# Kernel optimization log

Measured on AMD Instinct MI355X. Metric: run time of the kernel, lower is better.

Reference implementation:

```python
import jax, jax.numpy as jnp
import numpy as np

NUM_USERS = 100000
NUM_ITEMS = 50000
NUM_NODES = NUM_USERS + NUM_ITEMS
EMB = 64
NUM_EDGES = 2000000
BATCH = 16384


def setup_inputs() -> dict:
    key = jax.random.key(0)
    ks = jax.random.split(key, 9)

    def xavier(k, shape):
        fan_in, fan_out = shape[-2], shape[-1]
        lim = float(np.sqrt(6.0 / (fan_in + fan_out)))
        return jax.random.uniform(k, shape, jnp.float32, -lim, lim)

    user_table = xavier(ks[0], (NUM_USERS, EMB))
    item_table = xavier(ks[1], (NUM_ITEMS, EMB))
    # gat1: in=64, heads=4, out=64 -> W1 [64, 256]; a1 [4, 128]
    W1 = xavier(ks[2], (EMB, EMB * 4))
    a1 = xavier(ks[3], (4, 2 * EMB))
    # gat2: in=256, heads=1, out=64 -> W2 [256, 64]; a2 [1, 128]
    W2 = xavier(ks[4], (EMB * 4, EMB))
    a2 = xavier(ks[5], (1, 2 * EMB))

    edge_index = jax.random.randint(ks[6], (2, NUM_EDGES), 0, NUM_NODES, dtype=jnp.int32)
    user_ids = jax.random.randint(ks[7], (BATCH,), 0, NUM_USERS, dtype=jnp.int32)
    item_ids = jax.random.randint(ks[8], (BATCH,), 0, NUM_ITEMS, dtype=jnp.int32)
    return {
        "user_table": user_table, "item_table": item_table,
        "W1": W1, "a1": a1, "W2": W2, "a2": a2,
        "edge_index": edge_index, "user_ids": user_ids, "item_ids": item_ids,
    }


def gat_layer(x, W, a, num_heads, out_features, src, dst, concat):
    n = x.shape[0]
    h = (x @ W).reshape(n, num_heads, out_features)          # [N,H,F]
    # attention score: (cat(h_src,h_dst) * a).sum(-1) == h_src.a_l + h_dst.a_r
    a_l, a_r = a[:, :out_features], a[:, out_features:]
    e_src = jnp.einsum('nhf,hf->nh', h, a_l)                 # [N,H]
    e_dst = jnp.einsum('nhf,hf->nh', h, a_r)
    att = e_src[src] + e_dst[dst]                            # [E,H]
    att = jnp.where(att > 0, att, 0.2 * att)                 # LeakyReLU(0.2)
    att = jnp.exp(att - jnp.max(att))                        # global max, as in torch code
    att_sum = jax.ops.segment_sum(att, dst, num_segments=n)  # [N,H]
    att = att / (att_sum[dst] + 1e-8)
    msg = att[:, :, None] * h[src]                           # [E,H,F]
    out = jax.ops.segment_sum(msg, dst, num_segments=n)      # [N,H,F]
    return out.reshape(n, -1) if concat else out.mean(axis=1)


def reference(user_table, item_table, W1, a1, W2, a2, edge_index, user_ids, item_ids):
    src, dst = edge_index[0], edge_index[1]
    all_emb = jnp.concatenate([user_table, item_table], axis=0)  # [N,64]
    h = gat_layer(all_emb, W1, a1, 4, EMB, src, dst, concat=True)  # [N,256]
    h = jax.nn.elu(h)
    h = gat_layer(h, W2, a2, 1, EMB, src, dst, concat=False)       # [N,64]
    h = h + all_emb
    user_emb = h[:NUM_USERS]
    item_emb = h[NUM_USERS:]
    return jnp.sum(user_emb[user_ids] * item_emb[item_ids], axis=1)
```

## Files before the change

### kernel.cpp

```cpp
#include <hip/hip_runtime.h>
#include <cstdint>
#include <cstddef>

#define NUM_USERS 100000
#define NUM_ITEMS 50000
#define NUM_NODES 150000
#define NUM_EDGES 2000000
#define BATCH 16384
#define BSHIFT 8
#define NBUCK ((NUM_NODES + 255) >> BSHIFT)
#define PA_EDGES 8192
#define PA_BLOCKS ((NUM_EDGES + PA_EDGES - 1) / PA_EDGES)
#define NNPAD 150016
#define TBLK (NNPAD / 64)

typedef _Float16 hf8 __attribute__((ext_vector_type(8)));
typedef _Float16 hf4 __attribute__((ext_vector_type(4)));
typedef float fx4 __attribute__((ext_vector_type(4)));

__global__ void flag_kernel(const int* __restrict__ uid, const int* __restrict__ iid,
                            int* __restrict__ nodelist, int* __restrict__ bcnt,
                            int* __restrict__ gcnt) {
  int i = blockIdx.x * blockDim.x + threadIdx.x;
  if (i < NBUCK) bcnt[i] = 0;
  if (i < 2) gcnt[i] = 0;
  if (i < BATCH) {
    nodelist[2 * i] = uid[i];
    nodelist[2 * i + 1] = NUM_USERS + iid[i];
  }
}

__global__ __launch_bounds__(256) void bhist_kernel(const int* __restrict__ dst,
                                                    int* __restrict__ bcnt) {
  __shared__ int bh[NBUCK];
  int t = threadIdx.x;
  for (int u = t; u < NBUCK; u += 256) bh[u] = 0;
  __syncthreads();
  int base = blockIdx.x * PA_EDGES;
#pragma unroll
  for (int u = 0; u < PA_EDGES / 256; ++u) {
    int e = base + u * 256 + t;
    if (e < NUM_EDGES) atomicAdd(&bh[dst[e] >> BSHIFT], 1);
  }
  __syncthreads();
  for (int u = t; u < NBUCK; u += 256) {
    int v = bh[u];
    if (v) atomicAdd(&bcnt[u], v);
  }
}

__global__ void bscan_kernel(const int* __restrict__ bcnt, int* __restrict__ bbase,
                             int* __restrict__ bcursor, int* __restrict__ offsets) {
  __shared__ int sh[1024];
  int t = threadIdx.x;
  int v = (t < NBUCK) ? bcnt[t] : 0;
  sh[t] = v;
  __syncthreads();
  for (int off = 1; off < 1024; off <<= 1) {
    int x = (t >= off) ? sh[t - off] : 0;
    __syncthreads();
    sh[t] += x;
    __syncthreads();
  }
  if (t < NBUCK) {
    bbase[t] = sh[t] - v;
    bcursor[t] = sh[t] - v;
  }
  if (t == NBUCK - 1) {
    bbase[NBUCK] = sh[t];
    offsets[NUM_NODES] = sh[t];
  }
}

__global__ __launch_bounds__(256) void bpart_kernel(const int* __restrict__ src,
                                                    const int* __restrict__ dst,
                                                    int* __restrict__ bcursor,
                                                    int2* __restrict__ ebuf) {
  __shared__ int lcnt[NBUCK];
  __shared__ int lbase[NBUCK];
  int t = threadIdx.x;
  for (int u = t; u < NBUCK; u += 256) lcnt[u] = 0;
  __syncthreads();
  int base = blockIdx.x * PA_EDGES;
#pragma unroll
  for (int u = 0; u < PA_EDGES / 256; ++u) {
    int e = base + u * 256 + t;
    if (e < NUM_EDGES) atomicAdd(&lcnt[dst[e] >> BSHIFT], 1);
  }
  __syncthreads();
  for (int u = t; u < NBUCK; u += 256) {
    int v = lcnt[u];
    lbase[u] = v ? atomicAdd(&bcursor[u], v) : 0;
    lcnt[u] = 0;
  }
  __syncthreads();
#pragma unroll
  for (int u = 0; u < PA_EDGES / 256; ++u) {
    int e = base + u * 256 + t;
    if (e < NUM_EDGES) {
      int d = dst[e];
      int b = d >> BSHIFT;
      int p = lbase[b] + atomicAdd(&lcnt[b], 1);
      ebuf[p] = make_int2(src[e], d);
    }
  }
}

__global__ __launch_bounds__(256) void bcsr_kernel(const int2* __restrict__ ebuf,
                                                   const int* __restrict__ bbase,
                                                   int* __restrict__ offsets,
                                                   int* __restrict__ srcs) {
  __shared__ int ncnt[256];
  __shared__ int sh[256];
  __shared__ int lcur[256];
  int b = blockIdx.x;
  int t = threadIdx.x;
  int node0 = b << BSHIFT;
  int ebeg = bbase[b], eend = bbase[b + 1];
  ncnt[t] = 0;
  __syncthreads();
  for (int i = ebeg + t; i < eend; i += 256)
    atomicAdd(&ncnt[ebuf[i].y - node0], 1);
  __syncthreads();
  int v = ncnt[t];
  sh[t] = v;
  __syncthreads();
  for (int off = 1; off < 256; off <<= 1) {
    int x = (t >= off) ? sh[t - off] : 0;
    __syncthreads();
    sh[t] += x;
    __syncthreads();
  }
  int excl = ebeg + sh[t] - v;
  if (node0 + t < NUM_NODES) offsets[node0 + t] = excl;
  lcur[t] = excl;
  __syncthreads();
  for (int i = ebeg + t; i < eend; i += 256) {
    int2 ed = ebuf[i];
    int p = atomicAdd(&lcur[ed.y - node0], 1);
    srcs[p] = ed.x;
  }
}

__global__ __launch_bounds__(256) void dlist_kernel(
    const int* __restrict__ offsets, int* __restrict__ gcnt,
    int* __restrict__ Ls, int* __restrict__ Lm,
    _Float16* __restrict__ aXhi, _Float16* __restrict__ aXlo) {
  __shared__ int c0, c1, b0, b1;
  int t = threadIdx.x;
  int n = blockIdx.x * 256 + t;
  if (t == 0) { c0 = 0; c1 = 0; }
  __syncthreads();
  int cls = -1, rank = 0;
  if (n < NUM_NODES) {
    int deg = offsets[n + 1] - offsets[n];
    cls = (deg <= 16) ? 0 : 1;
    rank = atomicAdd(cls == 0 ? &c0 : &c1, 1);
  } else if (n < NNPAD) {
    float4 z = make_float4(0.f, 0.f, 0.f, 0.f);
#pragma unroll
    for (int i = 0; i < 32; ++i) {
      ((float4*)(aXhi + (size_t)n * 256))[i] = z;
      ((float4*)(aXlo + (size_t)n * 256))[i] = z;
    }
  }
  __syncthreads();
  if (t == 0) {
    b0 = atomicAdd(&gcnt[0], c0);
    b1 = atomicAdd(&gcnt[1], c1);
  }
  __syncthreads();
  if (cls == 0) Ls[b0 + rank] = n;
  else if (cls == 1) Lm[b1 + rank] = n;
}

__global__ void proj1_kernel(const float* __restrict__ W1, const float* __restrict__ a1,
                             float* __restrict__ w1a, float* __restrict__ w1b) {
  int t = threadIdx.x;
  int h = t >> 6, k = t & 63;
  float sa = 0.f, sb = 0.f;
  for (int f = 0; f < 64; ++f) {
    float w = W1[(size_t)k * 256 + h * 64 + f];
    sa += w * a1[h * 128 + f];
    sb += w * a1[h * 128 + 64 + f];
  }
  w1a[h * 64 + k] = sa;
  w1b[h * 64 + k] = sb;
}

__device__ __forceinline__ const float* row_ptr(int s, const float* __restrict__ ut,
                                                const float* __restrict__ it) {
  return (s < NUM_USERS) ? ut + (size_t)s * 64 : it + (size_t)(s - NUM_USERS) * 64;
}

__device__ __forceinline__ float lrexp(float x) {
  x = x > 0.f ? x : 0.2f * x;
  return __expf(x);
}

__device__ __forceinline__ float wnorm(float w) {
  float sum = w;
#pragma unroll
  for (int off = 32; off; off >>= 1) sum += __shfl_xor(sum, off, 64);
  return w * (1.f / (sum + 1e-8f));
}

__device__ __forceinline__ void fold4(float4& a) {
#pragma unroll
  for (int off = 16; off <= 32; off <<= 1) {
    a.x += __shfl_xor(a.x, off, 64);
    a.y += __shfl_xor(a.y, off, 64);
    a.z += __shfl_xor(a.z, off, 64);
    a.w += __shfl_xor(a.w, off, 64);
  }
}

__device__ __forceinline__ float elu(float x) {
  return x > 0.f ? x : (__expf(x) - 1.f);
}

__device__ __forceinline__ void split4(float4 o, hf4& hv, hf4& lv) {
  float a0 = o.x * 256.f, a1 = o.y * 256.f, a2 = o.z * 256.f, a3 = o.w * 256.f;
  _Float16 h0 = (_Float16)a0, h1 = (_Float16)a1;
  _Float16 h2 = (_Float16)a2, h3 = (_Float16)a3;
  hv[0] = h0; hv[1] = h1; hv[2] = h2; hv[3] = h3;
  lv[0] = (_Float16)(a0 - (float)h0);
  lv[1] = (_Float16)(a1 - (float)h1);
  lv[2] = (_Float16)(a2 - (float)h2);
  lv[3] = (_Float16)(a3 - (float)h3);
}

__device__ __forceinline__ void splitstore(_Float16* __restrict__ hi,
                                           _Float16* __restrict__ lo,
                                           size_t idx, float v) {
  v *= 256.f;
  _Float16 h = (_Float16)v;
  hi[idx] = h;
  lo[idx] = (_Float16)(v - (float)h);
}

__global__ __launch_bounds__(256) void e1g_kernel(
    const float* __restrict__ ut, const float* __restrict__ it,
    const float* __restrict__ w1a, const float* __restrict__ w1b,
    float* __restrict__ e1s, float* __restrict__ e1d) {
  int t = threadIdx.x;
  int wave = t >> 6, lane = t & 63;
  int g = lane >> 4, fl = lane & 15;
  int node = blockIdx.x * 16 + wave * 4 + g;
  bool valid = node < NUM_NODES;
  float4 xv = make_float4(0.f, 0.f, 0.f, 0.f);
  if (valid) xv = *(const float4*)(row_ptr(node, ut, it) + fl * 4);
  float ps[4], pd[4];
#pragma unroll
  for (int h = 0; h < 4; ++h) {
    float4 wa = *(const float4*)(w1a + h * 64 + fl * 4);
    float4 wb = *(const float4*)(w1b + h * 64 + fl * 4);
    ps[h] = xv.x * wa.x + xv.y * wa.y + xv.z * wa.z + xv.w * wa.w;
    pd[h] = xv.x * wb.x + xv.y * wb.y + xv.z * wb.z + xv.w * wb.w;
  }
#pragma unroll
  for (int off = 8; off; off >>= 1) {
#pragma unroll
    for (int h = 0; h < 4; ++h) {
      ps[h] += __shfl_xor(ps[h], off, 16);
      pd[h] += __shfl_xor(pd[h], off, 16);
    }
  }
  if (valid && fl == 0) {
    *(float4*)(e1s + (size_t)node * 4) = make_float4(ps[0], ps[1], ps[2], ps[3]);
    *(float4*)(e1d + (size_t)node * 4) = make_float4(pd[0], pd[1], pd[2], pd[3]);
  }
}

__global__ __launch_bounds__(256) void aggXs_kernel(
    const int* __restrict__ Ls, const int* __restrict__ gcnt,
    const int* __restrict__ offsets, const int* __restrict__ srcs,
    const float* __restrict__ e1s, const float* __restrict__ e1d,
    const float* __restrict__ ut, const float* __restrict__ it,
    _Float16* __restrict__ aXhi, _Float16* __restrict__ aXlo) {
  __shared__ int sS[4][68];
  __shared__ __align__(16) float4 sW[4][68];
  const int t = threadIdx.x;
  const int wave = t >> 6, lane = t & 63;
  const int g = lane >> 4, fl = lane & 15;
  const int cnt = gcnt[0];
  const int widx = blockIdx.x * 16 + wave * 4 + g;
  const int node = (widx < cnt) ? Ls[widx] : -1;

  int beg = 0, deg = 0;
  float4 ed = make_float4(0.f, 0.f, 0.f, 0.f);
  if (node >= 0) {
    beg = offsets[node];
    deg = offsets[node + 1] - beg;
    ed = *(const float4*)(e1d + (size_t)node * 4);
  }
  int s = 0;
  float w0 = 0.f, w1 = 0.f, w2 = 0.f, w3 = 0.f;
  if (fl < deg) {
    s = srcs[beg + fl];
    float4 ev = *(const float4*)(e1s + (size_t)s * 4);
    w0 = lrexp(ev.x + ed.x);
    w1 = lrexp(ev.y + ed.y);
    w2 = lrexp(ev.z + ed.z);
    w3 = lrexp(ev.w + ed.w);
  }
  float t0 = w0, t1 = w1, t2 = w2, t3 = w3;
#pragma unroll
  for (int off = 8; off; off >>= 1) {
    t0 += __shfl_xor(t0, off, 16);
    t1 += __shfl_xor(t1, off, 16);
    t2 += __shfl_xor(t2, off, 16);
    t3 += __shfl_xor(t3, off, 16);
  }
  w0 *= 1.f / (t0 + 1e-8f);
  w1 *= 1.f / (t1 + 1e-8f);
  w2 *= 1.f / (t2 + 1e-8f);
  w3 *= 1.f / (t3 + 1e-8f);
  sS[wave][g * 17 + fl] = s;
  sW[wave][g * 17 + fl] = make_float4(w0, w1, w2, w3);

  int md = deg;
  md = max(md, __shfl_xor(md, 16, 64));
  md = max(md, __shfl_xor(md, 32, 64));

  float4 a0 = make_float4(0.f, 0.f, 0.f, 0.f);
  float4 a1 = a0, a2 = a0, a3 = a0;
#pragma unroll 2
  for (int e = 0; e < md; ++e) {
    int se = sS[wave][g * 17 + e];
    float4 w4 = sW[wave][g * 17 + e];
    float4 xv = *(const float4*)(row_ptr(se, ut, it) + fl * 4);
    a0.x += w4.x * xv.x; a0.y += w4.x * xv.y; a0.z += w4.x * xv.z; a0.w += w4.x * xv.w;
    a1.x += w4.y * xv.x; a1.y += w4.y * xv.y; a1.z += w4.y * xv.z; a1.w += w4.y * xv.w;
    a2.x += w4.z * xv.x; a2.y += w4.z * xv.y; a2.z += w4.z * xv.z; a2.w += w4.z * xv.w;
    a3.x += w4.w * xv.x; a3.y += w4.w * xv.y; a3.z += w4.w * xv.z; a3.w += w4.w * xv.w;
  }
  if (node >= 0) {
    hf4 hv, lv;
    split4(a0, hv, lv);
    *(hf4*)(aXhi + (size_t)node * 256 + 0 * 64 + fl * 4) = hv;
    *(hf4*)(aXlo + (size_t)node * 256 + 0 * 64 + fl * 4) = lv;
    split4(a1, hv, lv);
    *(hf4*)(aXhi + (size_t)node * 256 + 1 * 64 + fl * 4) = hv;
    *(hf4*)(aXlo + (size_t)node * 256 + 1 * 64 + fl * 4) = lv;
    split4(a2, hv, lv);
    *(hf4*)(aXhi + (size_t)node * 256 + 2 * 64 + fl * 4) = hv;
    *(hf4*)(aXlo + (size_t)node * 256 + 2 * 64 + fl * 4) = lv;
    split4(a3, hv, lv);
    *(hf4*)(aXhi + (size_t)node * 256 + 3 * 64 + fl * 4) = hv;
    *(hf4*)(aXlo + (size_t)node * 256 + 3 * 64 + fl * 4) = lv;
  }
}

__global__ __launch_bounds__(256) void aggXm_kernel(
    const int* __restrict__ Lm, const int* __restrict__ gcnt,
    const int* __restrict__ offsets, const int* __restrict__ srcs,
    const float* __restrict__ e1s, const float* __restrict__ e1d,
    const float* __restrict__ ut, const float* __restrict__ it,
    _Float16* __restrict__ aXhi, _Float16* __restrict__ aXlo) {
  int wid = threadIdx.x >> 6, lane = threadIdx.x & 63;
  int idx = blockIdx.x * 4 + wid;
  if (idx >= gcnt[1]) return;
  int node = Lm[idx];
  int beg = offsets[node], end = offsets[node + 1];
  int deg = end - beg;

  float edv0 = e1d[(size_t)node * 4 + 0];
  float edv1 = e1d[(size_t)node * 4 + 1];
  float edv2 = e1d[(size_t)node * 4 + 2];
  float edv3 = e1d[(size_t)node * 4 + 3];

  if (deg <= 64) {
    int s = 0;
    float w0 = 0.f, w1 = 0.f, w2 = 0.f, w3 = 0.f;
    if (lane < deg) {
      s = srcs[beg + lane];
      float4 ev = *(const float4*)(e1s + (size_t)s * 4);
      w0 = lrexp(ev.x + edv0);
      w1 = lrexp(ev.y + edv1);
      w2 = lrexp(ev.z + edv2);
      w3 = lrexp(ev.w + edv3);
    }
    w0 = wnorm(w0);
    w1 = wnorm(w1);
    w2 = wnorm(w2);
    w3 = wnorm(w3);

    const int g = lane >> 4, fl = lane & 15;
    float4 acc0 = make_float4(0.f, 0.f, 0.f, 0.f);
    float4 acc1 = acc0, acc2 = acc0, acc3 = acc0;
#pragma unroll 4
    for (int e = 0; e < deg; e += 4) {
      int ei = e + g;
      int sg = __shfl(s, ei, 64);
      float4 xv = *(const float4*)(row_ptr(sg, ut, it) + fl * 4);
      float wg0 = __shfl(w0, ei, 64);
      acc0.x += wg0 * xv.x; acc0.y += wg0 * xv.y;
      acc0.z += wg0 * xv.z; acc0.w += wg0 * xv.w;
      float wg1 = __shfl(w1, ei, 64);
      acc1.x += wg1 * xv.x; acc1.y += wg1 * xv.y;
      acc1.z += wg1 * xv.z; acc1.w += wg1 * xv.w;
      float wg2 = __shfl(w2, ei, 64);
      acc2.x += wg2 * xv.x; acc2.y += wg2 * xv.y;
      acc2.z += wg2 * xv.z; acc2.w += wg2 * xv.w;
      float wg3 = __shfl(w3, ei, 64);
      acc3.x += wg3 * xv.x; acc3.y += wg3 * xv.y;
      acc3.z += wg3 * xv.z; acc3.w += wg3 * xv.w;
    }
    fold4(acc0); fold4(acc1); fold4(acc2); fold4(acc3);

    float4 o = (g == 0) ? acc0 : (g == 1) ? acc1 : (g == 2) ? acc2 : acc3;
    hf4 hv, lv;
    split4(o, hv, lv);
    *(hf4*)(aXhi + (size_t)node * 256 + lane * 4) = hv;
    *(hf4*)(aXlo + (size_t)node * 256 + lane * 4) = lv;
  } else {
    float s0 = 0.f, s1 = 0.f, s2 = 0.f, s3 = 0.f;
    for (int e = beg + lane; e < end; e += 64) {
      int s = srcs[e];
      float4 ev = *(const float4*)(e1s + (size_t)s * 4);
      s0 += lrexp(ev.x + edv0); s1 += lrexp(ev.y + edv1);
      s2 += lrexp(ev.z + edv2); s3 += lrexp(ev.w + edv3);
    }
#pragma unroll
    for (int off = 32; off; off >>= 1) {
      s0 += __shfl_xor(s0, off, 64);
      s1 += __shfl_xor(s1, off, 64);
      s2 += __shfl_xor(s2, off, 64);
      s3 += __shfl_xor(s3, off, 64);
    }
    float i0 = 1.f / (s0 + 1e-8f), i1 = 1.f / (s1 + 1e-8f);
    float i2 = 1.f / (s2 + 1e-8f), i3 = 1.f / (s3 + 1e-8f);
    float a0 = 0.f, a1 = 0.f, a2 = 0.f, a3 = 0.f;
    for (int e = beg; e < end; ++e) {
      int sn = srcs[e];
      float xv = row_ptr(sn, ut, it)[lane];
      float4 ev = *(const float4*)(e1s + (size_t)sn * 4);
      a0 += lrexp(ev.x + edv0) * i0 * xv;
      a1 += lrexp(ev.y + edv1) * i1 * xv;
      a2 += lrexp(ev.z + edv2) * i2 * xv;
      a3 += lrexp(ev.w + edv3) * i3 * xv;
    }
    splitstore(aXhi, aXlo, (size_t)node * 256 + 0 * 64 + lane, a0);
    splitstore(aXhi, aXlo, (size_t)node * 256 + 1 * 64 + lane, a1);
    splitstore(aXhi, aXlo, (size_t)node * 256 + 2 * 64 + lane, a2);
    splitstore(aXhi, aXlo, (size_t)node * 256 + 3 * 64 + lane, a3);
  }
}

__global__ void wprep_kernel(const float* __restrict__ W1, const float* __restrict__ W2,
                             _Float16* __restrict__ w1t_hi, _Float16* __restrict__ w1t_lo,
                             _Float16* __restrict__ w2t_hi, _Float16* __restrict__ w2t_lo) {
  int t = threadIdx.x;
  int h = t >> 6, a = t & 63;
  for (int k = 0; k < 64; ++k) {
    float w = W1[(size_t)k * 256 + h * 64 + a] * 256.f;
    _Float16 hi = (_Float16)w;
    w1t_hi[(size_t)(h * 64 + a) * 64 + k] = hi;
    w1t_lo[(size_t)(h * 64 + a) * 64 + k] = (_Float16)(w - (float)hi);

    float v = W2[(size_t)(h * 64 + k) * 64 + a] * 256.f;
    _Float16 hi2 = (_Float16)v;
    w2t_hi[(size_t)(h * 64 + a) * 64 + k] = hi2;
    w2t_lo[(size_t)(h * 64 + a) * 64 + k] = (_Float16)(v - (float)hi2);
  }
}

__device__ __forceinline__ fx4 mfma3(fx4 c, hf8 ah, hf8 al, hf8 bh, hf8 bl) {
  c = __builtin_amdgcn_mfma_f32_16x16x32_f16(ah, bh, c, 0, 0, 0);
  c = __builtin_amdgcn_mfma_f32_16x16x32_f16(al, bh, c, 0, 0, 0);
  c = __builtin_amdgcn_mfma_f32_16x16x32_f16(ah, bl, c, 0, 0, 0);
  return c;
}

__global__ __launch_bounds__(64, 2) void trans_mfma_kernel(
    const _Float16* __restrict__ aXhi, const _Float16* __restrict__ aXlo,
    const _Float16* __restrict__ w1t_hi, const _Float16* __restrict__ w1t_lo,
    const _Float16* __restrict__ w2t_hi, const _Float16* __restrict__ w2t_lo,
    const float* __restrict__ a2v,
    float* __restrict__ h2g, float* __restrict__ e2s, float* __restrict__ e2d) {
  __shared__ __align__(16) _Float16 t1hi[64 * 64];
  __shared__ __align__(16) _Float16 t1lo[64 * 64];
  const int l = threadIdx.x;
  const int lr = l & 15, lg = l >> 4;
  const int node0 = blockIdx.x * 64;
  const float DS = 1.52587890625e-05f;

  fx4 acc2[4][4];
#pragma unroll
  for (int m = 0; m < 4; ++m)
#pragma unroll
    for (int n = 0; n < 4; ++n) acc2[m][n] = (fx4){0.f, 0.f, 0.f, 0.f};

#pragma unroll 1
  for (int h = 0; h < 4; ++h) {
    fx4 acc1[4][4];
#pragma unroll
    for (int m = 0; m < 4; ++m)
#pragma unroll
      for (int n = 0; n < 4; ++n) acc1[m][n] = (fx4){0.f, 0.f, 0.f, 0.f};

#pragma unroll
    for (int ks = 0; ks < 2; ++ks) {
      const int ko = ks * 32 + lg * 8;
      hf8 wah[4], wal[4], xbh[4], xbl[4];
#pragma unroll
      for (int m = 0; m < 4; ++m) {
        size_t wo = (size_t)((h * 64 + m * 16 + lr) * 64 + ko);
        wah[m] = *(const hf8*)(w1t_hi + wo);
        wal[m] = *(const hf8*)(w1t_lo + wo);
      }
#pragma unroll
      for (int n = 0; n < 4; ++n) {
        size_t xo = (size_t)(node0 + n * 16 + lr) * 256 + h * 64 + ko;
        xbh[n] = *(const hf8*)(aXhi + xo);
        xbl[n] = *(const hf8*)(aXlo + xo);
      }
#pragma unroll
      for (int m = 0; m < 4; ++m)
#pragma unroll
        for (int n = 0; n < 4; ++n)
          acc1[m][n] = mfma3(acc1[m][n], wah[m], wal[m], xbh[n], xbl[n]);
    }

#pragma unroll
    for (int m = 0; m < 4; ++m)
#pragma unroll
      for (int n = 0; n < 4; ++n) {
        hf4 hv, lv;
#pragma unroll
        for (int r = 0; r < 4; ++r) {
          float v = acc1[m][n][r] * DS;
          v = elu(v) * 256.f;
          _Float16 hi = (_Float16)v;
          hv[r] = hi;
          lv[r] = (_Float16)(v - (float)hi);
        }
        int nl = n * 16 + lr;
        int ro = (m * 32 + lg * 8) ^ ((nl & 7) << 4);
        *(hf4*)((char*)t1hi + nl * 128 + ro) = hv;
        *(hf4*)((char*)t1lo + nl * 128 + ro) = lv;
      }

#pragma unroll
    for (int ks = 0; ks < 2; ++ks) {
      const int ko = ks * 32 + lg * 8;
      hf8 wah[4], wal[4], tbh[4], tbl[4];
#pragma unroll
      for (int m = 0; m < 4; ++m) {
        size_t wo = (size_t)((h * 64 + m * 16 + lr) * 64 + ko);
        wah[m] = *(const hf8*)(w2t_hi + wo);
        wal[m] = *(const hf8*)(w2t_lo + wo);
      }
#pragma unroll
      for (int n = 0; n < 4; ++n) {
        int nl = n * 16 + lr;
        int ro = (ks * 64 + lg * 16) ^ ((nl & 7) << 4);
        tbh[n] = *(const hf8*)((char*)t1hi + nl * 128 + ro);
        tbl[n] = *(const hf8*)((char*)t1lo + nl * 128 + ro);
      }
#pragma unroll
      for (int m = 0; m < 4; ++m)
#pragma unroll
        for (int n = 0; n < 4; ++n)
          acc2[m][n] = mfma3(acc2[m][n], wah[m], wal[m], tbh[n], tbl[n]);
    }
  }

  float ps[4] = {0.f, 0.f, 0.f, 0.f};
  float pd[4] = {0.f, 0.f, 0.f, 0.f};
#pragma unroll
  for (int m = 0; m < 4; ++m) {
    fx4 al = *(const fx4*)(a2v + m * 16 + lg * 4);
    fx4 ar = *(const fx4*)(a2v + 64 + m * 16 + lg * 4);
#pragma unroll
    for (int n = 0; n < 4; ++n) {
      fx4 v = acc2[m][n] * DS;
      int node = node0 + n * 16 + lr;
      if (node < NUM_NODES)
        *(fx4*)(h2g + (size_t)node * 64 + m * 16 + lg * 4) = v;
      ps[n] += v[0] * al[0] + v[1] * al[1] + v[2] * al[2] + v[3] * al[3];
      pd[n] += v[0] * ar[0] + v[1] * ar[1] + v[2] * ar[2] + v[3] * ar[3];
    }
  }
#pragma unroll
  for (int n = 0; n < 4; ++n) {
    float s = ps[n], d = pd[n];
    s += __shfl_xor(s, 16, 64);
    s += __shfl_xor(s, 32, 64);
    d += __shfl_xor(d, 16, 64);
    d += __shfl_xor(d, 32, 64);
    int node = node0 + n * 16 + lr;
    if (lg == n && node < NUM_NODES) {
      e2s[node] = s;
      e2d[node] = d;
    }
  }
}

__global__ __launch_bounds__(256) void agg2_kernel(
    const int* __restrict__ offsets, const int* __restrict__ srcs,
    const float* __restrict__ e2s, const float* __restrict__ e2d,
    const int* __restrict__ nodelist, const float* __restrict__ h2,
    const float* __restrict__ ut, const float* __restrict__ it,
    float* __restrict__ hfin) {
  int wid = threadIdx.x >> 6, lane = threadIdx.x & 63;
  int idx = blockIdx.x * 4 + wid;
  if (idx >= 2 * BATCH) return;
  int node = nodelist[idx];
  int beg = offsets[node], end = offsets[node + 1];
  int deg = end - beg;
  float edv = e2d[node];

  if (deg <= 64) {
    int s = 0;
    float w = 0.f;
    if (lane < deg) {
      s = srcs[beg + lane];
      w = lrexp(e2s[s] + edv);
    }
    w = wnorm(w);

    const int g = lane >> 4, fl = lane & 15;
    float4 acc = make_float4(0.f, 0.f, 0.f, 0.f);
#pragma unroll 4
    for (int e = 0; e < deg; e += 4) {
      int ei = e + g;
      int sg = __shfl(s, ei, 64);
      float wg = __shfl(w, ei, 64);
      float4 hv = *(const float4*)(h2 + (size_t)sg * 64 + fl * 4);
      acc.x += wg * hv.x; acc.y += wg * hv.y; acc.z += wg * hv.z; acc.w += wg * hv.w;
    }
    fold4(acc);
    if (g == 0) {
      const float* rp = (node < NUM_USERS) ? ut + (size_t)node * 64
                                           : it + (size_t)(node - NUM_USERS) * 64;
      float4 res = *(const float4*)(rp + fl * 4);
      acc.x += res.x; acc.y += res.y; acc.z += res.z; acc.w += res.w;
      *(float4*)(hfin + (size_t)node * 64 + fl * 4) = acc;
    }
  } else {
    float psum = 0.f;
    for (int e = beg + lane; e < end; e += 64) {
      int s = srcs[e];
      psum += lrexp(e2s[s] + edv);
    }
#pragma unroll
    for (int off = 32; off; off >>= 1) psum += __shfl_xor(psum, off, 64);
    float inv = 1.f / (psum + 1e-8f);
    float acc = 0.f;
    for (int e = beg; e < end; ++e) {
      int s0 = srcs[e];
      acc += lrexp(e2s[s0] + edv) * inv * h2[(size_t)s0 * 64 + lane];
    }
    float res = (node < NUM_USERS) ? ut[(size_t)node * 64 + lane]
                                   : it[(size_t)(node - NUM_USERS) * 64 + lane];
    hfin[(size_t)node * 64 + lane] = acc + res;
  }
}

__global__ __launch_bounds__(256) void final_kernel(
    const float* __restrict__ hf, const int* __restrict__ uid,
    const int* __restrict__ iid, float* __restrict__ out) {
  int wid = threadIdx.x >> 6, lane = threadIdx.x & 63;
  int idx = blockIdx.x * 4 + wid;
  if (idx >= BATCH) return;
  int u = uid[idx], v = iid[idx];
  float a = hf[(size_t)u * 64 + lane];
  float b = hf[(size_t)(NUM_USERS + v) * 64 + lane];
  float p = a * b;
#pragma unroll
  for (int off = 32; off; off >>= 1) p += __shfl_xor(p, off, 64);
  if (lane == 0) out[idx] = p;
}

extern "C" void kernel_launch(void* const* d_in, const int* in_sizes, int n_in,
                              void* d_out, int out_size, void* d_ws, size_t ws_size,
                              hipStream_t stream) {
  const float* user_table = (const float*)d_in[0];
  const float* item_table = (const float*)d_in[1];
  const float* W1 = (const float*)d_in[2];
  const float* a1 = (const float*)d_in[3];
  const float* W2 = (const float*)d_in[4];
  const float* a2 = (const float*)d_in[5];
  const int* edge_index = (const int*)d_in[6];
  const int* user_ids = (const int*)d_in[7];
  const int* item_ids = (const int*)d_in[8];
  float* out = (float*)d_out;

  const int* src = edge_index;
  const int* dst = edge_index + NUM_EDGES;

  float* ws = (float*)d_ws;
  size_t off = 0;
  auto falloc = [&](size_t n) { float* p = ws + off; off += n; return p; };
  float* h2  = falloc((size_t)NUM_NODES * 64);
  float* e1s = falloc((size_t)NUM_NODES * 4);
  float* e1d = falloc((size_t)NUM_NODES * 4);
  float* e2s = falloc(NUM_NODES);
  float* e2d = falloc(NUM_NODES);
  float* w1a = falloc(256);
  float* w1b = falloc(256);
  int* offsets  = (int*)falloc(NUM_NODES + 1);
  int* srcs     = (int*)falloc(NUM_EDGES);
  int* nodelist = (int*)falloc(2 * BATCH);
  int* bcnt     = (int*)falloc(NBUCK);
  int* bbase    = (int*)falloc(NBUCK + 1);
  int* bcursor  = (int*)falloc(NBUCK);
  int* gcnt     = (int*)falloc(2);
  int* Ls       = (int*)falloc(NNPAD);
  int* Lm       = (int*)falloc(NNPAD);
  off = (off + 3) & ~(size_t)3;
  _Float16* aggXhi = (_Float16*)(ws + off); off += (size_t)NNPAD * 128;
  _Float16* aggXlo = (_Float16*)(ws + off); off += (size_t)NNPAD * 128;

  int2* ebuf = (int2*)aggXhi;
  float* hfin = (float*)aggXhi;
  _Float16* w1t_hi = (_Float16*)falloc(4 * 64 * 64 / 2 + 16);
  _Float16* w1t_lo = (_Float16*)falloc(4 * 64 * 64 / 2 + 16);
  _Float16* w2t_hi = (_Float16*)falloc(4 * 64 * 64 / 2 + 16);
  _Float16* w2t_lo = (_Float16*)falloc(4 * 64 * 64 / 2 + 16);

  flag_kernel<<<(BATCH + 255) / 256, 256, 0, stream>>>(user_ids, item_ids,
                                                       nodelist, bcnt, gcnt);
  bhist_kernel<<<PA_BLOCKS, 256, 0, stream>>>(dst, bcnt);
  bscan_kernel<<<1, 1024, 0, stream>>>(bcnt, bbase, bcursor, offsets);
  bpart_kernel<<<PA_BLOCKS, 256, 0, stream>>>(src, dst, bcursor, ebuf);
  bcsr_kernel<<<NBUCK, 256, 0, stream>>>(ebuf, bbase, offsets, srcs);
  dlist_kernel<<<(NNPAD + 255) / 256, 256, 0, stream>>>(offsets, gcnt, Ls, Lm,
                                                        aggXhi, aggXlo);

  proj1_kernel<<<1, 256, 0, stream>>>(W1, a1, w1a, w1b);
  e1g_kernel<<<(NNPAD + 15) / 16, 256, 0, stream>>>(user_table, item_table,
                                                    w1a, w1b, e1s, e1d);

  aggXs_kernel<<<(NNPAD + 15) / 16, 256, 0, stream>>>(Ls, gcnt, offsets, srcs,
                                                      e1s, e1d, user_table,
                                                      item_table, aggXhi, aggXlo);
  aggXm_kernel<<<(NNPAD + 3) / 4, 256, 0, stream>>>(Lm, gcnt, offsets, srcs,
                                                    e1s, e1d, user_table,
                                                    item_table, aggXhi, aggXlo);
  wprep_kernel<<<1, 256, 0, stream>>>(W1, W2, w1t_hi, w1t_lo, w2t_hi, w2t_lo);
  trans_mfma_kernel<<<TBLK, 64, 0, stream>>>(aggXhi, aggXlo,
                                             w1t_hi, w1t_lo, w2t_hi, w2t_lo,
                                             a2, h2, e2s, e2d);

  agg2_kernel<<<(2 * BATCH + 3) / 4, 256, 0, stream>>>(offsets, srcs, e2s, e2d,
                                                       nodelist, h2,
                                                       user_table, item_table, hfin);
  final_kernel<<<(BATCH + 3) / 4, 256, 0, stream>>>(hfin, user_ids, item_ids, out);
}
```

Measured before the change: 499.4 us.

## Shrink per-wave tile to 32 nodes and pack four waves per block

The dense transform kernel now gives each wave 32 nodes instead of 64. It launches 256-thread blocks holding four waves, each with a private LDS slice. Weight fragments are loaded per m-iteration instead of all at once, which cuts accumulator and register pressure and allows more resident waves to hide latency. In exchange, each weight fragment is reused across fewer nodes, so weight loads per node double.

```diff
diff --git a/kernel.cpp b/kernel.cpp
--- a/kernel.cpp
+++ b/kernel.cpp
@@ -12,7 +12,7 @@
 #define PA_EDGES 8192
 #define PA_BLOCKS ((NUM_EDGES + PA_EDGES - 1) / PA_EDGES)
 #define NNPAD 150016
-#define TBLK (NNPAD / 64)
+#define TBLK2 (NNPAD / 128)
 
 typedef _Float16 hf8 __attribute__((ext_vector_type(8)));
 typedef _Float16 hf4 __attribute__((ext_vector_type(4)));
@@ -473,60 +473,61 @@
   return c;
 }
 
-__global__ __launch_bounds__(64, 2) void trans_mfma_kernel(
+__global__ __launch_bounds__(256, 4) void trans_mfma_kernel(
     const _Float16* __restrict__ aXhi, const _Float16* __restrict__ aXlo,
     const _Float16* __restrict__ w1t_hi, const _Float16* __restrict__ w1t_lo,
     const _Float16* __restrict__ w2t_hi, const _Float16* __restrict__ w2t_lo,
     const float* __restrict__ a2v,
     float* __restrict__ h2g, float* __restrict__ e2s, float* __restrict__ e2d) {
-  __shared__ __align__(16) _Float16 t1hi[64 * 64];
-  __shared__ __align__(16) _Float16 t1lo[64 * 64];
-  const int l = threadIdx.x;
+  __shared__ __align__(16) _Float16 t1hi[4][32 * 64];
+  __shared__ __align__(16) _Float16 t1lo[4][32 * 64];
+  const int wave = threadIdx.x >> 6;
+  const int l = threadIdx.x & 63;
   const int lr = l & 15, lg = l >> 4;
-  const int node0 = blockIdx.x * 64;
+  const int node0 = (blockIdx.x * 4 + wave) * 32;
+  char* myhi = (char*)&t1hi[wave][0];
+  char* mylo = (char*)&t1lo[wave][0];
   const float DS = 1.52587890625e-05f;
 
-  fx4 acc2[4][4];
+  fx4 acc2[4][2];
 #pragma unroll
   for (int m = 0; m < 4; ++m)
 #pragma unroll
-    for (int n = 0; n < 4; ++n) acc2[m][n] = (fx4){0.f, 0.f, 0.f, 0.f};
+    for (int n = 0; n < 2; ++n) acc2[m][n] = (fx4){0.f, 0.f, 0.f, 0.f};
 
 #pragma unroll 1
   for (int h = 0; h < 4; ++h) {
-    fx4 acc1[4][4];
+    fx4 acc1[4][2];
 #pragma unroll
     for (int m = 0; m < 4; ++m)
 #pragma unroll
-      for (int n = 0; n < 4; ++n) acc1[m][n] = (fx4){0.f, 0.f, 0.f, 0.f};
+      for (int n = 0; n < 2; ++n) acc1[m][n] = (fx4){0.f, 0.f, 0.f, 0.f};
 
 #pragma unroll
     for (int ks = 0; ks < 2; ++ks) {
       const int ko = ks * 32 + lg * 8;
-      hf8 wah[4], wal[4], xbh[4], xbl[4];
-#pragma unroll
-      for (int m = 0; m < 4; ++m) {
-        size_t wo = (size_t)((h * 64 + m * 16 + lr) * 64 + ko);
-        wah[m] = *(const hf8*)(w1t_hi + wo);
-        wal[m] = *(const hf8*)(w1t_lo + wo);
-      }
-#pragma unroll
-      for (int n = 0; n < 4; ++n) {
+      hf8 xbh[2], xbl[2];
+#pragma unroll
+      for (int n = 0; n < 2; ++n) {
         size_t xo = (size_t)(node0 + n * 16 + lr) * 256 + h * 64 + ko;
         xbh[n] = *(const hf8*)(aXhi + xo);
         xbl[n] = *(const hf8*)(aXlo + xo);
       }
 #pragma unroll
-      for (int m = 0; m < 4; ++m)
-#pragma unroll
-        for (int n = 0; n < 4; ++n)
-          acc1[m][n] = mfma3(acc1[m][n], wah[m], wal[m], xbh[n], xbl[n]);
+      for (int m = 0; m < 4; ++m) {
+        size_t wo = (size_t)((h * 64 + m * 16 + lr) * 64 + ko);
+        hf8 wah = *(const hf8*)(w1t_hi + wo);
+        hf8 wal = *(const hf8*)(w1t_lo + wo);
+#pragma unroll
+        for (int n = 0; n < 2; ++n)
+          acc1[m][n] = mfma3(acc1[m][n], wah, wal, xbh[n], xbl[n]);
+      }
     }
 
 #pragma unroll
     for (int m = 0; m < 4; ++m)
 #pragma unroll
-      for (int n = 0; n < 4; ++n) {
+      for (int n = 0; n < 2; ++n) {
         hf4 hv, lv;
 #pragma unroll
         for (int r = 0; r < 4; ++r) {
@@ -538,43 +539,41 @@
         }
         int nl = n * 16 + lr;
         int ro = (m * 32 + lg * 8) ^ ((nl & 7) << 4);
-        *(hf4*)((char*)t1hi + nl * 128 + ro) = hv;
-        *(hf4*)((char*)t1lo + nl * 128 + ro) = lv;
+        *(hf4*)(myhi + nl * 128 + ro) = hv;
+        *(hf4*)(mylo + nl * 128 + ro) = lv;
       }
 
 #pragma unroll
     for (int ks = 0; ks < 2; ++ks) {
       const int ko = ks * 32 + lg * 8;
-      hf8 wah[4], wal[4], tbh[4], tbl[4];
+      hf8 tbh[2], tbl[2];
+#pragma unroll
+      for (int n = 0; n < 2; ++n) {
+        int nl = n * 16 + lr;
+        int ro = (ks * 64 + lg * 16) ^ ((nl & 7) << 4);
+        tbh[n] = *(const hf8*)(myhi + nl * 128 + ro);
+        tbl[n] = *(const hf8*)(mylo + nl * 128 + ro);
+      }
 #pragma unroll
       for (int m = 0; m < 4; ++m) {
         size_t wo = (size_t)((h * 64 + m * 16 + lr) * 64 + ko);
-        wah[m] = *(const hf8*)(w2t_hi + wo);
-        wal[m] = *(const hf8*)(w2t_lo + wo);
+        hf8 wah = *(const hf8*)(w2t_hi + wo);
+        hf8 wal = *(const hf8*)(w2t_lo + wo);
+#pragma unroll
+        for (int n = 0; n < 2; ++n)
+          acc2[m][n] = mfma3(acc2[m][n], wah, wal, tbh[n], tbl[n]);
       }
-#pragma unroll
-      for (int n = 0; n < 4; ++n) {
-        int nl = n * 16 + lr;
-        int ro = (ks * 64 + lg * 16) ^ ((nl & 7) << 4);
-        tbh[n] = *(const hf8*)((char*)t1hi + nl * 128 + ro);
-        tbl[n] = *(const hf8*)((char*)t1lo + nl * 128 + ro);
-      }
-#pragma unroll
-      for (int m = 0; m < 4; ++m)
-#pragma unroll
-        for (int n = 0; n < 4; ++n)
-          acc2[m][n] = mfma3(acc2[m][n], wah[m], wal[m], tbh[n], tbl[n]);
-    }
-  }
-
-  float ps[4] = {0.f, 0.f, 0.f, 0.f};
-  float pd[4] = {0.f, 0.f, 0.f, 0.f};
+    }
+  }
+
+  float ps[2] = {0.f, 0.f};
+  float pd[2] = {0.f, 0.f};
 #pragma unroll
   for (int m = 0; m < 4; ++m) {
     fx4 al = *(const fx4*)(a2v + m * 16 + lg * 4);
     fx4 ar = *(const fx4*)(a2v + 64 + m * 16 + lg * 4);
 #pragma unroll
-    for (int n = 0; n < 4; ++n) {
+    for (int n = 0; n < 2; ++n) {
       fx4 v = acc2[m][n] * DS;
       int node = node0 + n * 16 + lr;
       if (node < NUM_NODES)
@@ -584,7 +583,7 @@
     }
   }
 #pragma unroll
-  for (int n = 0; n < 4; ++n) {
+  for (int n = 0; n < 2; ++n) {
     float s = ps[n], d = pd[n];
     s += __shfl_xor(s, 16, 64);
     s += __shfl_xor(s, 32, 64);
@@ -741,9 +740,9 @@
                                                     e1s, e1d, user_table,
                                                     item_table, aggXhi, aggXlo);
   wprep_kernel<<<1, 256, 0, stream>>>(W1, W2, w1t_hi, w1t_lo, w2t_hi, w2t_lo);
-  trans_mfma_kernel<<<TBLK, 64, 0, stream>>>(aggXhi, aggXlo,
-                                             w1t_hi, w1t_lo, w2t_hi, w2t_lo,
-                                             a2, h2, e2s, e2d);
+  trans_mfma_kernel<<<TBLK2, 256, 0, stream>>>(aggXhi, aggXlo,
+                                               w1t_hi, w1t_lo, w2t_hi, w2t_lo,
+                                               a2, h2, e2s, e2d);
 
   agg2_kernel<<<(2 * BATCH + 3) / 4, 256, 0, stream>>>(offsets, srcs, e2s, e2d,
                                                        nodelist, h2,
```

Measured after the change: 571.9 us. +14.5%, slower.
